# Performance work log

Hardware: AMD Instinct MI355X
Metric: run time of the kernel (lower is better)

The kernel has to match this reference:

```python
import jax, jax.numpy as jnp
import numpy as np

EPS = 1e-5

def layer_norm(x, gamma, beta):
    m = jnp.mean(x, axis=-1, keepdims=True)
    v = jnp.var(x, axis=-1, keepdims=True)
    return (x - m) / jnp.sqrt(v + EPS) * gamma + beta


def setup_inputs() -> dict:
    key = jax.random.key(0)
    ks = jax.random.split(key, 10)
    B, N, D = 2, 2048, 1024
    H, Dh = 16, 64
    C, CD = 256, 512
    inner = H * Dh  # 1024
    J = C + 1 + N  # 2305 = context + null + self

    x = jax.random.normal(ks[0], (B, N, D), dtype=jnp.float32)
    context = jax.random.normal(ks[1], (B, C, CD), dtype=jnp.float32)
    mask = jax.random.uniform(ks[2], (B, C + N)) < 0.9  # bool, mostly True
    attn_bias = jax.random.normal(ks[3], (H, N, J), dtype=jnp.float32) * 0.02

    norm_gamma = jnp.ones((D,), dtype=jnp.float32)
    null_kv = jax.random.normal(ks[4], (2, Dh), dtype=jnp.float32)
    Wq = jax.random.normal(ks[5], (D, inner), dtype=jnp.float32) * (D ** -0.5)
    Wkv = jax.random.normal(ks[6], (D, 2 * Dh), dtype=jnp.float32) * (D ** -0.5)
    ctx_ln_w = jnp.ones((CD,), dtype=jnp.float32)
    ctx_ln_b = jnp.zeros((CD,), dtype=jnp.float32)
    Wctx = jax.random.normal(ks[7], (CD, 2 * Dh), dtype=jnp.float32) * (CD ** -0.5)
    bctx = jnp.zeros((2 * Dh,), dtype=jnp.float32)
    Wout = jax.random.normal(ks[8], (inner, D), dtype=jnp.float32) * (inner ** -0.5)
    out_gamma = jnp.ones((D,), dtype=jnp.float32)

    return {"x": x, "context": context, "mask": mask, "attn_bias": attn_bias,
            "norm_gamma": norm_gamma, "null_kv": null_kv, "Wq": Wq, "Wkv": Wkv,
            "ctx_ln_w": ctx_ln_w, "ctx_ln_b": ctx_ln_b, "Wctx": Wctx, "bctx": bctx,
            "Wout": Wout, "out_gamma": out_gamma}


def reference(x, context, mask, attn_bias, norm_gamma, null_kv, Wq, Wkv,
              ctx_ln_w, ctx_ln_b, Wctx, bctx, Wout, out_gamma):
    B, N, D = x.shape
    Dh = null_kv.shape[-1]
    H = Wq.shape[-1] // Dh
    scale = Dh ** -0.5

    xn = layer_norm(x, norm_gamma, 0.0)
    q = (xn @ Wq).reshape(B, N, H, Dh).transpose(0, 2, 1, 3) * scale  # b h n d
    k, v = jnp.split(xn @ Wkv, 2, axis=-1)  # b n d each (multi-query: shared across heads)

    # prepend learned null kv token
    nk = jnp.broadcast_to(null_kv[0], (B, 1, Dh))
    nv = jnp.broadcast_to(null_kv[1], (B, 1, Dh))
    k = jnp.concatenate([nk, k], axis=1)
    v = jnp.concatenate([nv, v], axis=1)

    # prepend projected context tokens
    cn = layer_norm(context, ctx_ln_w, ctx_ln_b)
    ck, cv = jnp.split(cn @ Wctx + bctx, 2, axis=-1)
    k = jnp.concatenate([ck, k], axis=1)  # b j d, j = C + 1 + N
    v = jnp.concatenate([cv, v], axis=1)

    sim = jnp.einsum('bhid,bjd->bhij', q, k) + attn_bias
    # pad mask with True for the null token (left), then broadcast over h, i
    m = jnp.pad(mask, ((0, 0), (1, 0)), constant_values=True)[:, None, None, :]
    max_neg = -jnp.finfo(sim.dtype).max
    sim = jnp.where(m, sim, max_neg)

    attn = jax.nn.softmax(sim.astype(jnp.float32), axis=-1)
    out = jnp.einsum('bhij,bjd->bhid', attn, v)  # b h n d
    out = out.transpose(0, 2, 1, 3).reshape(B, N, H * Dh)
    return layer_norm(out @ Wout, out_gamma, 0.0)
```

## Files before the change

kernel.cpp:

```cpp
#include <hip/hip_runtime.h>

constexpr int B  = 2;
constexpr int N  = 2048;
constexpr int H  = 16;
constexpr int C  = 256;
constexpr int J  = C + 1 + N;
constexpr int Jp = 2368;
constexpr int NT = Jp / 64;
constexpr float EPS = 1e-5f;
constexpr float LOG2E = 1.4426950408889634f;

typedef __bf16 bf16x8 __attribute__((ext_vector_type(8)));
typedef float  f32x4  __attribute__((ext_vector_type(4)));
typedef unsigned int uint4v __attribute__((ext_vector_type(4)));
typedef __attribute__((address_space(3))) unsigned int lds_u32;
typedef const __attribute__((address_space(1))) unsigned int glb_u32;

__device__ inline void load_lds16(const void* g, void* l) {
    __builtin_amdgcn_global_load_lds((glb_u32*)g, (lds_u32*)l, 16, 0, 0);
}
__device__ inline unsigned short f2bf(float f) {
    unsigned int u = __builtin_bit_cast(unsigned int, f);
    u += 0x7fffu + ((u >> 16) & 1u);
    return (unsigned short)(u >> 16);
}
__device__ inline unsigned int packbf2(float a, float b) {
    union { __bf16 h[2]; unsigned int u; } cv;
    cv.h[0] = (__bf16)a;
    cv.h[1] = (__bf16)b;
    return cv.u;
}
__device__ inline float fexp2(float x) {
    float r;
    asm("v_exp_f32 %0, %1" : "=v"(r) : "v"(x));
    return r;
}
__device__ inline f32x4 mfma16(bf16x8 a, bf16x8 b, f32x4 c) {
    return __builtin_amdgcn_mfma_f32_16x16x32_bf16(a, b, c, 0, 0, 0);
}
__device__ inline f32x4 loadu4(const float* p) {
    f32x4 r;
    __builtin_memcpy(&r, p, 16);
    return r;
}

__global__ void mask_prep(const void* __restrict__ mraw, float* __restrict__ maskf) {
    __shared__ int bad_int, bad_f32;
    const int t = threadIdx.x;
    if (t == 0) { bad_int = 0; bad_f32 = 0; }
    __syncthreads();
    const unsigned int* w = (const unsigned int*)mraw;
    int li = 0, lf = 0;
    for (int i = t; i < 1152; i += 256) {
        unsigned int v = w[i];
        if (v > 1u) li = 1;
        if (v != 0u && v != 0x3F800000u) lf = 1;
    }
    if (li) atomicOr(&bad_int, 1);
    if (lf) atomicOr(&bad_f32, 1);
    __syncthreads();
    const int mode = (!bad_int) ? 0 : ((!bad_f32) ? 1 : 2);
    const unsigned char* bytes = (const unsigned char*)mraw;
    for (int i = t; i < 2 * Jp; i += 256) {
        const int b2 = i / Jp, jp = i - b2 * Jp;
        float v;
        if (jp == 0) v = 0.f;
        else if (jp >= J) v = -1e30f;
        else {
            const int idx = b2 * (C + N) + jp - 1;
            const int keep = (mode == 2) ? (bytes[idx] != 0) : (w[idx] != 0u);
            v = keep ? 0.f : -1e30f;
        }
        maskf[i] = v;
    }
}

__global__ void zero_pads(unsigned short* __restrict__ Kb, unsigned short* __restrict__ Vt) {
    const int t = threadIdx.x;
    for (int i = t; i < 2 * 63 * 64; i += 256) {
        const int b2 = i / (63 * 64);
        const int rr = (i / 64) % 63;
        const int d  = i % 64;
        Kb[(size_t)(b2 * Jp + J + rr) * 64 + d] = 0;
    }
    for (int i = t; i < 2 * 64 * 63; i += 256) {
        const int b2 = i / (64 * 63);
        const int d  = (i / 63) % 64;
        const int cc = i % 63;
        Vt[(size_t)(b2 * 64 + d) * Jp + J + cc] = 0;
    }
}

template <int BF16OUT>
__global__ void __launch_bounds__(256) ln1024(const float* __restrict__ x,
                                              const float* __restrict__ gamma,
                                              void* __restrict__ outp) {
    const int row = blockIdx.x;
    const int t = threadIdx.x;
    const float* xr = x + (size_t)row * 1024;
    float4 v = ((const float4*)xr)[t];
    float s  = v.x + v.y + v.z + v.w;
    float ss = v.x * v.x + v.y * v.y + v.z * v.z + v.w * v.w;
    #pragma unroll
    for (int o = 1; o < 64; o <<= 1) {
        s  += __shfl_xor(s, o);
        ss += __shfl_xor(ss, o);
    }
    __shared__ float red[8];
    const int w = t >> 6;
    if ((t & 63) == 0) { red[w * 2] = s; red[w * 2 + 1] = ss; }
    __syncthreads();
    s  = red[0] + red[2] + red[4] + red[6];
    ss = red[1] + red[3] + red[5] + red[7];
    const float mean = s * (1.0f / 1024.0f);
    const float var  = ss * (1.0f / 1024.0f) - mean * mean;
    const float rstd = rsqrtf(var + EPS);
    const float4 g = ((const float4*)gamma)[t];
    float o0 = (v.x - mean) * rstd * g.x;
    float o1 = (v.y - mean) * rstd * g.y;
    float o2 = (v.z - mean) * rstd * g.z;
    float o3 = (v.w - mean) * rstd * g.w;
    if (BF16OUT) {
        ushort4 u;
        u.x = f2bf(o0); u.y = f2bf(o1); u.z = f2bf(o2); u.w = f2bf(o3);
        *(ushort4*)((unsigned short*)outp + (size_t)row * 1024 + t * 4) = u;
    } else {
        *(float4*)((float*)outp + (size_t)row * 1024 + t * 4) = make_float4(o0, o1, o2, o3);
    }
}

__global__ void __launch_bounds__(256) transpose_w(const float* __restrict__ W,
                                                   unsigned short* __restrict__ WT,
                                                   int K, int Nn, float scale) {
    __shared__ float lds[64][68];
    const int k0 = blockIdx.x * 64, n0 = blockIdx.y * 64;
    const int t = threadIdx.x;
    const int kk = t >> 4, nn = (t & 15) * 4;
    #pragma unroll
    for (int r = 0; r < 4; r++) {
        const float4 v = *(const float4*)(W + (size_t)(k0 + kk + r * 16) * Nn + n0 + nn);
        lds[kk + r * 16][nn + 0] = v.x;
        lds[kk + r * 16][nn + 1] = v.y;
        lds[kk + r * 16][nn + 2] = v.z;
        lds[kk + r * 16][nn + 3] = v.w;
    }
    __syncthreads();
    const int nr = t >> 2, kc = (t & 3) * 16;
    #pragma unroll
    for (int u4 = 0; u4 < 4; u4++) {
        ushort4 u;
        u.x = f2bf(lds[kc + u4 * 4 + 0][nr] * scale);
        u.y = f2bf(lds[kc + u4 * 4 + 1][nr] * scale);
        u.z = f2bf(lds[kc + u4 * 4 + 2][nr] * scale);
        u.w = f2bf(lds[kc + u4 * 4 + 3][nr] * scale);
        *(ushort4*)(WT + (size_t)(n0 + nr) * K + k0 + kc + u4 * 4) = u;
    }
}

__global__ void __launch_bounds__(128) ctx_proj(const float* __restrict__ ctx,
                                                const float* __restrict__ lw,
                                                const float* __restrict__ lb,
                                                const float* __restrict__ Wc,
                                                const float* __restrict__ bc,
                                                unsigned short* __restrict__ Kb,
                                                unsigned short* __restrict__ Vt) {
    const int row = blockIdx.x;
    const int b2 = row >> 8, ci = row & 255;
    const int t = threadIdx.x;
    __shared__ float cn[512];
    __shared__ float red[4];
    const float* xr = ctx + (size_t)row * 512;
    float4 v = ((const float4*)xr)[t];
    float s  = v.x + v.y + v.z + v.w;
    float ss = v.x * v.x + v.y * v.y + v.z * v.z + v.w * v.w;
    #pragma unroll
    for (int o = 1; o < 64; o <<= 1) {
        s  += __shfl_xor(s, o);
        ss += __shfl_xor(ss, o);
    }
    const int w = t >> 6;
    if ((t & 63) == 0) { red[w * 2] = s; red[w * 2 + 1] = ss; }
    __syncthreads();
    s  = red[0] + red[2];
    ss = red[1] + red[3];
    const float mean = s * (1.0f / 512.0f);
    const float var  = ss * (1.0f / 512.0f) - mean * mean;
    const float rstd = rsqrtf(var + EPS);
    const float4 g  = ((const float4*)lw)[t];
    const float4 be = ((const float4*)lb)[t];
    float4 c4;
    c4.x = (v.x - mean) * rstd * g.x + be.x;
    c4.y = (v.y - mean) * rstd * g.y + be.y;
    c4.z = (v.z - mean) * rstd * g.z + be.z;
    c4.w = (v.w - mean) * rstd * g.w + be.w;
    *(float4*)&cn[t * 4] = c4;
    __syncthreads();
    float acc = bc[t];
    #pragma unroll 8
    for (int d = 0; d < 512; d++) acc = fmaf(cn[d], Wc[d * 128 + t], acc);
    const unsigned short bv = f2bf(acc);
    if (t < 64) Kb[(size_t)(b2 * Jp + ci) * 64 + t] = bv;
    else        Vt[(size_t)(b2 * 64 + (t - 64)) * Jp + ci] = bv;
}

__global__ void null_fill(const float* __restrict__ nkv,
                          unsigned short* __restrict__ Kb, unsigned short* __restrict__ Vt) {
    const int b2 = blockIdx.x;
    const int t = threadIdx.x;
    Kb[(size_t)(b2 * Jp + 256) * 64 + t] = f2bf(nkv[t]);
    Vt[(size_t)(b2 * 64 + t) * Jp + 256] = f2bf(nkv[64 + t]);
}

template <int MODE>
__global__ void __launch_bounds__(256, 2) gemm_bf16(
        const unsigned short* __restrict__ A, const unsigned short* __restrict__ BT,
        float* __restrict__ Cf, unsigned short* __restrict__ Cb,
        unsigned short* __restrict__ Kb, unsigned short* __restrict__ Vt,
        int M, int Nn, int K) {
    __shared__ __align__(16) unsigned char smem[65536];
    const int t = threadIdx.x;
    const int w = t >> 6, lane = t & 63;
    const int g = lane >> 4, ln15 = lane & 15;
    const int wm = w >> 1, wn = w & 1;
    const int row0 = blockIdx.x * 128, col0 = blockIdx.y * 128;
    const int nk = K >> 6;
    const int ls = lane >> 3;
    const int swz = (lane & 7) ^ ls;

    f32x4 acc[4][4];
    #pragma unroll
    for (int i = 0; i < 4; i++)
        #pragma unroll
        for (int jj = 0; jj < 4; jj++)
            acc[i][jj] = (f32x4){0.f, 0.f, 0.f, 0.f};

    auto stage = [&](int kt, int cur) {
        if (w < 2) {
            const unsigned short* src = A + (size_t)(row0 + w * 64 + ls) * K + kt * 64 + swz * 8;
            unsigned char* dst = smem + cur * 16384 + w * 8192;
            #pragma unroll
            for (int i = 0; i < 8; i++)
                load_lds16(src + (size_t)i * 8 * K, dst + i * 1024);
        } else {
            const unsigned short* src = BT + (size_t)(col0 + (w - 2) * 64 + ls) * K + kt * 64 + swz * 8;
            unsigned char* dst = smem + 32768 + cur * 16384 + (w - 2) * 8192;
            #pragma unroll
            for (int i = 0; i < 8; i++)
                load_lds16(src + (size_t)i * 8 * K, dst + i * 1024);
        }
    };

    stage(0, 0);
    __syncthreads();
    for (int kt = 0; kt < nk; kt++) {
        const int cur = kt & 1;
        if (kt + 1 < nk) stage(kt + 1, cur ^ 1);
        const unsigned char* As = smem + cur * 16384;
        const unsigned char* Bs = smem + 32768 + cur * 16384;
        #pragma unroll
        for (int ks = 0; ks < 2; ks++) {
            bf16x8 af[4], bf[4];
            #pragma unroll
            for (int mq = 0; mq < 4; mq++)
                af[mq] = *(const bf16x8*)(As + (wm * 64 + mq * 16 + ln15) * 128 +
                                          ((ks * 64 + g * 16) ^ ((ln15 & 7) << 4)));
            #pragma unroll
            for (int nq = 0; nq < 4; nq++)
                bf[nq] = *(const bf16x8*)(Bs + (wn * 64 + nq * 16 + ln15) * 128 +
                                          ((ks * 64 + g * 16) ^ ((ln15 & 7) << 4)));
            #pragma unroll
            for (int mq = 0; mq < 4; mq++)
                #pragma unroll
                for (int nq = 0; nq < 4; nq++)
                    acc[mq][nq] = mfma16(af[mq], bf[nq], acc[mq][nq]);
        }
        __syncthreads();
    }

    #pragma unroll
    for (int mq = 0; mq < 4; mq++) {
        #pragma unroll
        for (int nq = 0; nq < 4; nq++) {
            #pragma unroll
            for (int r = 0; r < 4; r++) {
                const int gr = row0 + wm * 64 + mq * 16 + g * 4 + r;
                const int gc = col0 + wn * 64 + nq * 16 + ln15;
                if (MODE == 0) {
                    Cf[(size_t)gr * Nn + gc] = acc[mq][nq][r];
                } else if (MODE == 1) {
                    Cb[(size_t)gr * Nn + gc] = f2bf(acc[mq][nq][r]);
                } else {
                    const int b2 = gr >> 11, tok = gr & 2047;
                    const unsigned short v = f2bf(acc[mq][nq][r]);
                    if (gc < 64) Kb[(size_t)(b2 * Jp + 257 + tok) * 64 + gc] = v;
                    else         Vt[(size_t)(b2 * 64 + gc - 64) * Jp + 257 + tok] = v;
                }
            }
        }
    }
}

__global__ void __launch_bounds__(1024, 4) attn_v8(
        const unsigned short* __restrict__ qb, const unsigned short* __restrict__ Kb,
        const unsigned short* __restrict__ Vt, const float* __restrict__ bias,
        const float* __restrict__ maskf, unsigned short* __restrict__ aout) {
    __shared__ __align__(16) unsigned char smem[135168];
    const int t = threadIdx.x;
    const int w = t >> 6, lane = t & 63;
    const int g = lane >> 4, ln15 = lane & 15;
    const int i0 = blockIdx.x * 128, h = blockIdx.y;
    const int b2 = w & 1, wq = w >> 1;
    const int ls = lane >> 3;
    const int swz = (lane & 7) ^ ls;

    auto stage = [&](int jt, int cur) {
        const int j0 = jt * 64;
        const int quarter = w & 3;
        if (w < 8) {
            const int kb = (w >> 2) & 1;
            const unsigned short* src = Kb + (size_t)(kb * Jp + j0 + quarter * 16 + ls) * 64 + swz * 8;
            unsigned char* dst = smem + cur * 32768 + kb * 8192 + quarter * 2048;
            load_lds16(src, dst);
            load_lds16(src + (size_t)8 * 64, dst + 1024);
        } else {
            const int vb = (w >> 2) & 1;
            const unsigned short* src = Vt + (size_t)(vb * 64 + quarter * 16 + ls) * Jp + j0 + swz * 8;
            unsigned char* dst = smem + cur * 32768 + 16384 + vb * 8192 + quarter * 2048;
            load_lds16(src, dst);
            load_lds16(src + (size_t)8 * Jp, dst + 1024);
        }
    };

    const int bq  = t >> 3;
    const int bs0 = t & 7;
    const float* biasQrow = bias + ((size_t)h * N + i0 + bq) * J;
    auto bias_issue = [&](int jt, f32x4& r0, f32x4& r1) {
        const int j0 = jt * 64;
        if (j0 + 64 <= J) {
            r0 = loadu4(biasQrow + j0 + bs0 * 4);
            r1 = loadu4(biasQrow + j0 + (bs0 + 8) * 4);
        } else {
            #pragma unroll
            for (int c = 0; c < 4; c++) {
                const int jA = j0 + bs0 * 4 + c;
                const int jB = j0 + (bs0 + 8) * 4 + c;
                r0[c] = (jA < J) ? biasQrow[jA] : 0.f;
                r1[c] = (jB < J) ? biasQrow[jB] : 0.f;
            }
        }
    };
    auto bias_write = [&](int cur, const f32x4& r0, const f32x4& r1) {
        float* basep = (float*)(smem + 65536 + cur * 34816) + bq * 68;
        *(f32x4*)(basep + bs0 * 4) = r0;
        *(f32x4*)(basep + (bs0 + 8) * 4) = r1;
    };

    bf16x8 qf[2];
    #pragma unroll
    for (int ks = 0; ks < 2; ks++)
        qf[ks] = *(const bf16x8*)(qb + (size_t)(b2 * N + i0 + wq * 16 + ln15) * 1024 +
                                  h * 64 + ks * 32 + g * 8);

    float mrun = -1e30f, lrun = 0.f;
    f32x4 outA[4];
    #pragma unroll
    for (int nq = 0; nq < 4; nq++) outA[nq] = (f32x4){0.f, 0.f, 0.f, 0.f};

    const int srclA = ln15 + (((2 * g + 0) & 3) << 4);
    const int srclB = ln15 + (((2 * g + 1) & 3) << 4);

    auto compute = [&](int jt, int cur) {
        const int j0 = jt * 64;
        const unsigned char* Kl = smem + cur * 32768 + b2 * 8192;
        const unsigned char* Vl = smem + cur * 32768 + 16384 + b2 * 8192;
        const float* bb = (const float*)(smem + 65536 + cur * 34816) + (wq * 16 + ln15) * 68;

        f32x4 mk[4];
        #pragma unroll
        for (int jqm = 0; jqm < 4; jqm++)
            mk[jqm] = *(const f32x4*)(maskf + b2 * Jp + j0 + jqm * 16 + g * 4);
        f32x4 br[4];
        #pragma unroll
        for (int jqm = 0; jqm < 4; jqm++)
            br[jqm] = *(const f32x4*)(bb + (jqm * 4 + g) * 4);

        f32x4 S[4];
        #pragma unroll
        for (int jqm = 0; jqm < 4; jqm++) S[jqm] = (f32x4){0.f, 0.f, 0.f, 0.f};
        #pragma unroll
        for (int ks = 0; ks < 2; ks++) {
            bf16x8 ka[4];
            #pragma unroll
            for (int jqm = 0; jqm < 4; jqm++)
                ka[jqm] = *(const bf16x8*)(Kl + (jqm * 16 + ln15) * 128 +
                                           ((ks * 64 + g * 16) ^ ((ln15 & 7) << 4)));
            __builtin_amdgcn_s_setprio(1);
            #pragma unroll
            for (int jqm = 0; jqm < 4; jqm++)
                S[jqm] = mfma16(ka[jqm], qf[ks], S[jqm]);
            __builtin_amdgcn_s_setprio(0);
        }

        float sv[4][4];
        #pragma unroll
        for (int jqm = 0; jqm < 4; jqm++)
            #pragma unroll
            for (int r = 0; r < 4; r++)
                sv[jqm][r] = fmaf(br[jqm][r], LOG2E, S[jqm][r]) + mk[jqm][r];

        float tmj[4];
        #pragma unroll
        for (int jqm = 0; jqm < 4; jqm++)
            tmj[jqm] = fmaxf(fmaxf(sv[jqm][0], sv[jqm][1]), fmaxf(sv[jqm][2], sv[jqm][3]));
        float tm = fmaxf(fmaxf(tmj[0], tmj[1]), fmaxf(tmj[2], tmj[3]));
        tm = fmaxf(tm, __shfl_xor(tm, 16));
        tm = fmaxf(tm, __shfl_xor(tm, 32));

        if (!__all(tm <= mrun)) {
            const float mnew = fmaxf(mrun, tm);
            const float cor = fexp2(mrun - mnew);
            mrun = mnew;
            float corr[4];
            #pragma unroll
            for (int r = 0; r < 4; r++) corr[r] = __shfl(cor, g * 4 + r, 64);
            #pragma unroll
            for (int nq = 0; nq < 4; nq++)
                #pragma unroll
                for (int r = 0; r < 4; r++)
                    outA[nq][r] *= corr[r];
            lrun *= cor;
        }
        const float mcur = mrun;

        float p[4][4];
        #pragma unroll
        for (int jqm = 0; jqm < 4; jqm++)
            #pragma unroll
            for (int r = 0; r < 4; r++)
                p[jqm][r] = fexp2(sv[jqm][r] - mcur);
        float tsj[4];
        #pragma unroll
        for (int jqm = 0; jqm < 4; jqm++)
            tsj[jqm] = (p[jqm][0] + p[jqm][1]) + (p[jqm][2] + p[jqm][3]);
        float ts = (tsj[0] + tsj[1]) + (tsj[2] + tsj[3]);
        ts += __shfl_xor(ts, 16);
        ts += __shfl_xor(ts, 32);
        lrun += ts;

        unsigned int Wp[4][2];
        #pragma unroll
        for (int jqm = 0; jqm < 4; jqm++) {
            Wp[jqm][0] = packbf2(p[jqm][0], p[jqm][1]);
            Wp[jqm][1] = packbf2(p[jqm][2], p[jqm][3]);
        }

        #pragma unroll
        for (int ks = 0; ks < 2; ks++) {
            uint4v wd;
            #pragma unroll
            for (int widx = 0; widx < 4; widx++) {
                const int srcl = (widx >> 1) ? srclB : srclA;
                const int t0 = __shfl((int)Wp[ks * 2 + 0][widx & 1], srcl, 64);
                const int t1 = __shfl((int)Wp[ks * 2 + 1][widx & 1], srcl, 64);
                wd[widx] = (unsigned int)((g >> 1) ? t1 : t0);
            }
            const bf16x8 pa = __builtin_bit_cast(bf16x8, wd);
            bf16x8 vf[4];
            #pragma unroll
            for (int nq = 0; nq < 4; nq++)
                vf[nq] = *(const bf16x8*)(Vl + (nq * 16 + ln15) * 128 +
                                          ((ks * 64 + g * 16) ^ ((ln15 & 7) << 4)));
            __builtin_amdgcn_s_setprio(1);
            #pragma unroll
            for (int nq = 0; nq < 4; nq++)
                outA[nq] = mfma16(pa, vf[nq], outA[nq]);
            __builtin_amdgcn_s_setprio(0);
        }
    };

    f32x4 bR0, bR1;
    bias_issue(0, bR0, bR1);
    stage(0, 0);
    bias_write(0, bR0, bR1);
    __syncthreads();
    for (int jt = 0; jt < NT; jt++) {
        const int cur = jt & 1;
        if (jt + 1 < NT) {
            bias_issue(jt + 1, bR0, bR1);
            stage(jt + 1, cur ^ 1);
        }
        compute(jt, cur);
        if (jt + 1 < NT) bias_write(cur ^ 1, bR0, bR1);
        __syncthreads();
    }

    const float inv = 1.0f / lrun;
    float invr[4];
    #pragma unroll
    for (int r = 0; r < 4; r++) invr[r] = __shfl(inv, g * 4 + r, 64);
    #pragma unroll
    for (int nq = 0; nq < 4; nq++)
        #pragma unroll
        for (int r = 0; r < 4; r++)
            aout[(size_t)(b2 * N + i0 + wq * 16 + g * 4 + r) * 1024 +
                 h * 64 + nq * 16 + ln15] = f2bf(outA[nq][r] * invr[r]);
}

extern "C" void kernel_launch(void* const* d_in, const int* in_sizes, int n_in,
                              void* d_out, int out_size, void* d_ws, size_t ws_size,
                              hipStream_t stream) {
    const float* x         = (const float*)d_in[0];
    const float* context   = (const float*)d_in[1];
    const void*  mask      = d_in[2];
    const float* bias      = (const float*)d_in[3];
    const float* norm_g    = (const float*)d_in[4];
    const float* null_kv   = (const float*)d_in[5];
    const float* Wq        = (const float*)d_in[6];
    const float* Wkv       = (const float*)d_in[7];
    const float* ctx_ln_w  = (const float*)d_in[8];
    const float* ctx_ln_b  = (const float*)d_in[9];
    const float* Wctx      = (const float*)d_in[10];
    const float* bctx      = (const float*)d_in[11];
    const float* Wout      = (const float*)d_in[12];
    const float* out_gamma = (const float*)d_in[13];
    float* out = (float*)d_out;

    unsigned char* wsb = (unsigned char*)d_ws;
    unsigned short* xnb   = (unsigned short*)(wsb + 0);
    unsigned short* qbb   = (unsigned short*)(wsb + 8388608);
    float*          y     = (float*)(wsb + 0);
    unsigned short* aoutp = (unsigned short*)(wsb + 16777216);
    unsigned short* KbP   = (unsigned short*)(wsb + 25165824);
    unsigned short* VtP   = (unsigned short*)(wsb + 25772032);
    float*          maskf = (float*)(wsb + 26378240);
    unsigned short* WqT   = (unsigned short*)(wsb + 26397184);
    unsigned short* WkvT  = (unsigned short*)(wsb + 28494336);
    unsigned short* WoutT = (unsigned short*)(wsb + 28756480);

    mask_prep<<<1, 256, 0, stream>>>(mask, maskf);
    zero_pads<<<1, 256, 0, stream>>>(KbP, VtP);
    ln1024<1><<<B * N, 256, 0, stream>>>(x, norm_g, xnb);
    transpose_w<<<dim3(16, 16), 256, 0, stream>>>(Wq, WqT, 1024, 1024, 0.125f * LOG2E);
    transpose_w<<<dim3(16, 2), 256, 0, stream>>>(Wkv, WkvT, 1024, 128, 1.0f);
    transpose_w<<<dim3(16, 16), 256, 0, stream>>>(Wout, WoutT, 1024, 1024, 1.0f);
    ctx_proj<<<B * C, 128, 0, stream>>>(context, ctx_ln_w, ctx_ln_b, Wctx, bctx, KbP, VtP);
    null_fill<<<B, 64, 0, stream>>>(null_kv, KbP, VtP);
    gemm_bf16<1><<<dim3(32, 8), 256, 0, stream>>>(xnb, WqT, nullptr, qbb, nullptr, nullptr, 4096, 1024, 1024);
    gemm_bf16<2><<<dim3(32, 1), 256, 0, stream>>>(xnb, WkvT, nullptr, nullptr, KbP, VtP, 4096, 128, 1024);
    attn_v8<<<dim3(16, 16), 1024, 0, stream>>>(qbb, KbP, VtP, bias, maskf, aoutp);
    gemm_bf16<0><<<dim3(32, 8), 256, 0, stream>>>(aoutp, WoutT, y, nullptr, nullptr, nullptr, 4096, 1024, 1024);
    ln1024<0><<<B * N, 256, 0, stream>>>(y, out_gamma, out);
}
```

Measured before the change: 252.2 us.

## Halve attention block to 8 waves, each wave processing two query tiles

The attention kernel now launches 512 threads instead of 1024, and each wave handles 32 query rows (two 16-row tiles) instead of 16. Each K and V fragment read from LDS feeds two MFMAs, and the staging and bias-load work is spread over fewer threads with more loads each. The aim is to cut LDS traffic per MFMA and raise per-wave instruction-level parallelism. In exchange it doubles accumulator and score register use per wave and halves the number of waves per block, which can reduce latency hiding.

Measured after the change: 273.6 us. 1.09x slower.

```diff
diff --git a/kernel.cpp b/kernel.cpp
--- a/kernel.cpp
+++ b/kernel.cpp
@@ -300,7 +300,7 @@
     }
 }
 
-__global__ void __launch_bounds__(1024, 4) attn_v8(
+__global__ void __launch_bounds__(512, 2) attn_v9(
         const unsigned short* __restrict__ qb, const unsigned short* __restrict__ Kb,
         const unsigned short* __restrict__ Vt, const float* __restrict__ bias,
         const float* __restrict__ maskf, unsigned short* __restrict__ aout) {
@@ -315,56 +315,71 @@
 
     auto stage = [&](int jt, int cur) {
         const int j0 = jt * 64;
-        const int quarter = w & 3;
-        if (w < 8) {
-            const int kb = (w >> 2) & 1;
-            const unsigned short* src = Kb + (size_t)(kb * Jp + j0 + quarter * 16 + ls) * 64 + swz * 8;
-            unsigned char* dst = smem + cur * 32768 + kb * 8192 + quarter * 2048;
-            load_lds16(src, dst);
-            load_lds16(src + (size_t)8 * 64, dst + 1024);
+        const int half = w & 1;
+        if (w < 4) {
+            const int kb = w >> 1;
+            const unsigned short* src = Kb + (size_t)(kb * Jp + j0 + half * 32 + ls) * 64 + swz * 8;
+            unsigned char* dst = smem + cur * 32768 + kb * 8192 + half * 4096;
+            #pragma unroll
+            for (int i = 0; i < 4; i++)
+                load_lds16(src + (size_t)i * 8 * 64, dst + i * 1024);
         } else {
-            const int vb = (w >> 2) & 1;
-            const unsigned short* src = Vt + (size_t)(vb * 64 + quarter * 16 + ls) * Jp + j0 + swz * 8;
-            unsigned char* dst = smem + cur * 32768 + 16384 + vb * 8192 + quarter * 2048;
-            load_lds16(src, dst);
-            load_lds16(src + (size_t)8 * Jp, dst + 1024);
+            const int vb = (w - 4) >> 1;
+            const unsigned short* src = Vt + (size_t)(vb * 64 + half * 32 + ls) * Jp + j0 + swz * 8;
+            unsigned char* dst = smem + cur * 32768 + 16384 + vb * 8192 + half * 4096;
+            #pragma unroll
+            for (int i = 0; i < 4; i++)
+                load_lds16(src + (size_t)i * 8 * Jp, dst + i * 1024);
         }
     };
 
-    const int bq  = t >> 3;
-    const int bs0 = t & 7;
+    const int bq  = t >> 2;
+    const int bs0 = (t & 3) * 16;
     const float* biasQrow = bias + ((size_t)h * N + i0 + bq) * J;
-    auto bias_issue = [&](int jt, f32x4& r0, f32x4& r1) {
+    auto bias_issue = [&](int jt, f32x4& r0, f32x4& r1, f32x4& r2, f32x4& r3) {
         const int j0 = jt * 64;
         if (j0 + 64 <= J) {
-            r0 = loadu4(biasQrow + j0 + bs0 * 4);
-            r1 = loadu4(biasQrow + j0 + (bs0 + 8) * 4);
+            r0 = loadu4(biasQrow + j0 + bs0 + 0);
+            r1 = loadu4(biasQrow + j0 + bs0 + 4);
+            r2 = loadu4(biasQrow + j0 + bs0 + 8);
+            r3 = loadu4(biasQrow + j0 + bs0 + 12);
         } else {
             #pragma unroll
             for (int c = 0; c < 4; c++) {
-                const int jA = j0 + bs0 * 4 + c;
-                const int jB = j0 + (bs0 + 8) * 4 + c;
-                r0[c] = (jA < J) ? biasQrow[jA] : 0.f;
-                r1[c] = (jB < J) ? biasQrow[jB] : 0.f;
+                const int ja = j0 + bs0 + c;
+                r0[c] = (ja      < J) ? biasQrow[ja]      : 0.f;
+                r1[c] = (ja + 4  < J) ? biasQrow[ja + 4]  : 0.f;
+                r2[c] = (ja + 8  < J) ? biasQrow[ja + 8]  : 0.f;
+                r3[c] = (ja + 12 < J) ? biasQrow[ja + 12] : 0.f;
             }
         }
     };
-    auto bias_write = [&](int cur, const f32x4& r0, const f32x4& r1) {
-        float* basep = (float*)(smem + 65536 + cur * 34816) + bq * 68;
-        *(f32x4*)(basep + bs0 * 4) = r0;
-        *(f32x4*)(basep + (bs0 + 8) * 4) = r1;
+    auto bias_write = [&](int cur, const f32x4& r0, const f32x4& r1,
+                          const f32x4& r2, const f32x4& r3) {
+        float* basep = (float*)(smem + 65536 + cur * 34816) + bq * 68 + bs0;
+        *(f32x4*)(basep + 0)  = r0;
+        *(f32x4*)(basep + 4)  = r1;
+        *(f32x4*)(basep + 8)  = r2;
+        *(f32x4*)(basep + 12) = r3;
     };
 
-    bf16x8 qf[2];
-    #pragma unroll
-    for (int ks = 0; ks < 2; ks++)
-        qf[ks] = *(const bf16x8*)(qb + (size_t)(b2 * N + i0 + wq * 16 + ln15) * 1024 +
-                                  h * 64 + ks * 32 + g * 8);
-
-    float mrun = -1e30f, lrun = 0.f;
-    f32x4 outA[4];
-    #pragma unroll
-    for (int nq = 0; nq < 4; nq++) outA[nq] = (f32x4){0.f, 0.f, 0.f, 0.f};
+    bf16x8 qf[2][2];
+    #pragma unroll
+    for (int qq = 0; qq < 2; qq++)
+        #pragma unroll
+        for (int ks = 0; ks < 2; ks++)
+            qf[qq][ks] = *(const bf16x8*)(qb +
+                (size_t)(b2 * N + i0 + wq * 32 + qq * 16 + ln15) * 1024 +
+                h * 64 + ks * 32 + g * 8);
+
+    float mrun[2] = {-1e30f, -1e30f};
+    float lrun[2] = {0.f, 0.f};
+    f32x4 outA[2][4];
+    #pragma unroll
+    for (int qq = 0; qq < 2; qq++)
+        #pragma unroll
+        for (int nq = 0; nq < 4; nq++)
+            outA[qq][nq] = (f32x4){0.f, 0.f, 0.f, 0.f};
 
     const int srclA = ln15 + (((2 * g + 0) & 3) << 4);
     const int srclB = ln15 + (((2 * g + 1) & 3) << 4);
@@ -373,20 +388,19 @@
         const int j0 = jt * 64;
         const unsigned char* Kl = smem + cur * 32768 + b2 * 8192;
         const unsigned char* Vl = smem + cur * 32768 + 16384 + b2 * 8192;
-        const float* bb = (const float*)(smem + 65536 + cur * 34816) + (wq * 16 + ln15) * 68;
+        const float* bbase = (const float*)(smem + 65536 + cur * 34816);
 
         f32x4 mk[4];
         #pragma unroll
         for (int jqm = 0; jqm < 4; jqm++)
             mk[jqm] = *(const f32x4*)(maskf + b2 * Jp + j0 + jqm * 16 + g * 4);
-        f32x4 br[4];
-        #pragma unroll
-        for (int jqm = 0; jqm < 4; jqm++)
-            br[jqm] = *(const f32x4*)(bb + (jqm * 4 + g) * 4);
-
-        f32x4 S[4];
-        #pragma unroll
-        for (int jqm = 0; jqm < 4; jqm++) S[jqm] = (f32x4){0.f, 0.f, 0.f, 0.f};
+
+        f32x4 S[2][4];
+        #pragma unroll
+        for (int qq = 0; qq < 2; qq++)
+            #pragma unroll
+            for (int jqm = 0; jqm < 4; jqm++)
+                S[qq][jqm] = (f32x4){0.f, 0.f, 0.f, 0.f};
         #pragma unroll
         for (int ks = 0; ks < 2; ks++) {
             bf16x8 ka[4];
@@ -396,75 +410,87 @@
                                            ((ks * 64 + g * 16) ^ ((ln15 & 7) << 4)));
             __builtin_amdgcn_s_setprio(1);
             #pragma unroll
-            for (int jqm = 0; jqm < 4; jqm++)
-                S[jqm] = mfma16(ka[jqm], qf[ks], S[jqm]);
+            for (int jqm = 0; jqm < 4; jqm++) {
+                S[0][jqm] = mfma16(ka[jqm], qf[0][ks], S[0][jqm]);
+                S[1][jqm] = mfma16(ka[jqm], qf[1][ks], S[1][jqm]);
+            }
             __builtin_amdgcn_s_setprio(0);
         }
 
-        float sv[4][4];
-        #pragma unroll
-        for (int jqm = 0; jqm < 4; jqm++)
-            #pragma unroll
-            for (int r = 0; r < 4; r++)
-                sv[jqm][r] = fmaf(br[jqm][r], LOG2E, S[jqm][r]) + mk[jqm][r];
-
-        float tmj[4];
-        #pragma unroll
-        for (int jqm = 0; jqm < 4; jqm++)
-            tmj[jqm] = fmaxf(fmaxf(sv[jqm][0], sv[jqm][1]), fmaxf(sv[jqm][2], sv[jqm][3]));
-        float tm = fmaxf(fmaxf(tmj[0], tmj[1]), fmaxf(tmj[2], tmj[3]));
-        tm = fmaxf(tm, __shfl_xor(tm, 16));
-        tm = fmaxf(tm, __shfl_xor(tm, 32));
-
-        if (!__all(tm <= mrun)) {
-            const float mnew = fmaxf(mrun, tm);
-            const float cor = fexp2(mrun - mnew);
-            mrun = mnew;
-            float corr[4];
-            #pragma unroll
-            for (int r = 0; r < 4; r++) corr[r] = __shfl(cor, g * 4 + r, 64);
-            #pragma unroll
-            for (int nq = 0; nq < 4; nq++)
+        unsigned int Wp[2][4][2];
+        #pragma unroll
+        for (int qq = 0; qq < 2; qq++) {
+            const float* bb = bbase + (wq * 32 + qq * 16 + ln15) * 68;
+            float sv[4][4];
+            #pragma unroll
+            for (int jqm = 0; jqm < 4; jqm++) {
+                const f32x4 br = *(const f32x4*)(bb + jqm * 16 + g * 4);
                 #pragma unroll
                 for (int r = 0; r < 4; r++)
-                    outA[nq][r] *= corr[r];
-            lrun *= cor;
-        }
-        const float mcur = mrun;
-
-        float p[4][4];
-        #pragma unroll
-        for (int jqm = 0; jqm < 4; jqm++)
-            #pragma unroll
-            for (int r = 0; r < 4; r++)
-                p[jqm][r] = fexp2(sv[jqm][r] - mcur);
-        float tsj[4];
-        #pragma unroll
-        for (int jqm = 0; jqm < 4; jqm++)
-            tsj[jqm] = (p[jqm][0] + p[jqm][1]) + (p[jqm][2] + p[jqm][3]);
-        float ts = (tsj[0] + tsj[1]) + (tsj[2] + tsj[3]);
-        ts += __shfl_xor(ts, 16);
-        ts += __shfl_xor(ts, 32);
-        lrun += ts;
-
-        unsigned int Wp[4][2];
-        #pragma unroll
-        for (int jqm = 0; jqm < 4; jqm++) {
-            Wp[jqm][0] = packbf2(p[jqm][0], p[jqm][1]);
-            Wp[jqm][1] = packbf2(p[jqm][2], p[jqm][3]);
+                    sv[jqm][r] = fmaf(br[r], LOG2E, S[qq][jqm][r]) + mk[jqm][r];
+            }
+
+            float tmj[4];
+            #pragma unroll
+            for (int jqm = 0; jqm < 4; jqm++)
+                tmj[jqm] = fmaxf(fmaxf(sv[jqm][0], sv[jqm][1]), fmaxf(sv[jqm][2], sv[jqm][3]));
+            float tm = fmaxf(fmaxf(tmj[0], tmj[1]), fmaxf(tmj[2], tmj[3]));
+            tm = fmaxf(tm, __shfl_xor(tm, 16));
+            tm = fmaxf(tm, __shfl_xor(tm, 32));
+
+            if (!__all(tm <= mrun[qq])) {
+                const float mnew = fmaxf(mrun[qq], tm);
+                const float cor = fexp2(mrun[qq] - mnew);
+                mrun[qq] = mnew;
+                float corr[4];
+                #pragma unroll
+                for (int r = 0; r < 4; r++) corr[r] = __shfl(cor, g * 4 + r, 64);
+                #pragma unroll
+                for (int nq = 0; nq < 4; nq++)
+                    #pragma unroll
+                    for (int r = 0; r < 4; r++)
+                        outA[qq][nq][r] *= corr[r];
+                lrun[qq] *= cor;
+            }
+            const float mcur = mrun[qq];
+
+            float p[4][4];
+            #pragma unroll
+            for (int jqm = 0; jqm < 4; jqm++)
+                #pragma unroll
+                for (int r = 0; r < 4; r++)
+                    p[jqm][r] = fexp2(sv[jqm][r] - mcur);
+            float tsj[4];
+            #pragma unroll
+            for (int jqm = 0; jqm < 4; jqm++)
+                tsj[jqm] = (p[jqm][0] + p[jqm][1]) + (p[jqm][2] + p[jqm][3]);
+            float ts = (tsj[0] + tsj[1]) + (tsj[2] + tsj[3]);
+            ts += __shfl_xor(ts, 16);
+            ts += __shfl_xor(ts, 32);
+            lrun[qq] += ts;
+
+            #pragma unroll
+            for (int jqm = 0; jqm < 4; jqm++) {
+                Wp[qq][jqm][0] = packbf2(p[jqm][0], p[jqm][1]);
+                Wp[qq][jqm][1] = packbf2(p[jqm][2], p[jqm][3]);
+            }
         }
 
         #pragma unroll
         for (int ks = 0; ks < 2; ks++) {
-            uint4v wd;
-            #pragma unroll
-            for (int widx = 0; widx < 4; widx++) {
-                const int srcl = (widx >> 1) ? srclB : srclA;
-                const int t0 = __shfl((int)Wp[ks * 2 + 0][widx & 1], srcl, 64);
-                const int t1 = __shfl((int)Wp[ks * 2 + 1][widx & 1], srcl, 64);
-                wd[widx] = (unsigned int)((g >> 1) ? t1 : t0);
-            }
-            const bf16x8 pa = __builtin_bit_cast(bf16x8, wd);
+            bf16x8 pa[2];
+            #pragma unroll
+            for (int qq = 0; qq < 2; qq++) {
+                uint4v wd;
+                #pragma unroll
+                for (int widx = 0; widx < 4; widx++) {
+                    const int srcl = (widx >> 1) ? srclB : srclA;
+                    const int t0 = __shfl((int)Wp[qq][ks * 2 + 0][widx & 1], srcl, 64);
+                    const int t1 = __shfl((int)Wp[qq][ks * 2 + 1][widx & 1], srcl, 64);
+                    wd[widx] = (unsigned int)((g >> 1) ? t1 : t0);
+                }
+                pa[qq] = __builtin_bit_cast(bf16x8, wd);
+            }
             bf16x8 vf[4];
             #pragma unroll
             for (int nq = 0; nq < 4; nq++)
@@ -472,38 +498,43 @@
                                           ((ks * 64 + g * 16) ^ ((ln15 & 7) << 4)));
             __builtin_amdgcn_s_setprio(1);
             #pragma unroll
-            for (int nq = 0; nq < 4; nq++)
-                outA[nq] = mfma16(pa, vf[nq], outA[nq]);
+            for (int nq = 0; nq < 4; nq++) {
+                outA[0][nq] = mfma16(pa[0], vf[nq], outA[0][nq]);
+                outA[1][nq] = mfma16(pa[1], vf[nq], outA[1][nq]);
+            }
             __builtin_amdgcn_s_setprio(0);
         }
     };
 
-    f32x4 bR0, bR1;
-    bias_issue(0, bR0, bR1);
+    f32x4 bR0, bR1, bR2, bR3;
+    bias_issue(0, bR0, bR1, bR2, bR3);
     stage(0, 0);
-    bias_write(0, bR0, bR1);
+    bias_write(0, bR0, bR1, bR2, bR3);
     __syncthreads();
     for (int jt = 0; jt < NT; jt++) {
         const int cur = jt & 1;
         if (jt + 1 < NT) {
-            bias_issue(jt + 1, bR0, bR1);
+            bias_issue(jt + 1, bR0, bR1, bR2, bR3);
             stage(jt + 1, cur ^ 1);
         }
         compute(jt, cur);
-        if (jt + 1 < NT) bias_write(cur ^ 1, bR0, bR1);
+        if (jt + 1 < NT) bias_write(cur ^ 1, bR0, bR1, bR2, bR3);
         __syncthreads();
     }
 
-    const float inv = 1.0f / lrun;
-    float invr[4];
-    #pragma unroll
-    for (int r = 0; r < 4; r++) invr[r] = __shfl(inv, g * 4 + r, 64);
-    #pragma unroll
-    for (int nq = 0; nq < 4; nq++)
-        #pragma unroll
-        for (int r = 0; r < 4; r++)
-            aout[(size_t)(b2 * N + i0 + wq * 16 + g * 4 + r) * 1024 +
-                 h * 64 + nq * 16 + ln15] = f2bf(outA[nq][r] * invr[r]);
+    #pragma unroll
+    for (int qq = 0; qq < 2; qq++) {
+        const float inv = 1.0f / lrun[qq];
+        float invr[4];
+        #pragma unroll
+        for (int r = 0; r < 4; r++) invr[r] = __shfl(inv, g * 4 + r, 64);
+        #pragma unroll
+        for (int nq = 0; nq < 4; nq++)
+            #pragma unroll
+            for (int r = 0; r < 4; r++)
+                aout[(size_t)(b2 * N + i0 + wq * 32 + qq * 16 + g * 4 + r) * 1024 +
+                     h * 64 + nq * 16 + ln15] = f2bf(outA[qq][nq][r] * invr[r]);
+    }
 }
 
 extern "C" void kernel_launch(void* const* d_in, const int* in_sizes, int n_in,
@@ -547,7 +578,7 @@
     null_fill<<<B, 64, 0, stream>>>(null_kv, KbP, VtP);
     gemm_bf16<1><<<dim3(32, 8), 256, 0, stream>>>(xnb, WqT, nullptr, qbb, nullptr, nullptr, 4096, 1024, 1024);
     gemm_bf16<2><<<dim3(32, 1), 256, 0, stream>>>(xnb, WkvT, nullptr, nullptr, KbP, VtP, 4096, 128, 1024);
-    attn_v8<<<dim3(16, 16), 1024, 0, stream>>>(qbb, KbP, VtP, bias, maskf, aoutp);
+    attn_v9<<<dim3(16, 16), 512, 0, stream>>>(qbb, KbP, VtP, bias, maskf, aoutp);
     gemm_bf16<0><<<dim3(32, 8), 256, 0, stream>>>(aoutp, WoutT, y, nullptr, nullptr, nullptr, 4096, 1024, 1024);
     ln1024<0><<<B * N, 256, 0, stream>>>(y, out_gamma, out);
 }
```

## Single-buffer attention LDS for two blocks per CU; merge small prep kernels

Applied to the files above, without the earlier changes.

The attention kernel drops its double-buffered K/V/bias staging in LDS and uses one buffer, halving shared memory so two 1024-thread blocks can be resident per CU. In exchange, loads for the next tile no longer overlap compute within a block, and an extra barrier is added per tile. Latency hiding now depends on the second resident block. Separately, the mask prep, pad zeroing and null-KV fill kernels are merged into one three-block launch to cut launch overhead.

New measurement: 770.3 us. +205.4%, slower.

```diff
diff --git a/kernel.cpp b/kernel.cpp
--- a/kernel.cpp
+++ b/kernel.cpp
@@ -44,50 +44,57 @@
     return r;
 }
 
-__global__ void mask_prep(const void* __restrict__ mraw, float* __restrict__ maskf) {
-    __shared__ int bad_int, bad_f32;
+__global__ void prep_all(const void* __restrict__ mraw, float* __restrict__ maskf,
+                         unsigned short* __restrict__ Kb, unsigned short* __restrict__ Vt,
+                         const float* __restrict__ nkv) {
     const int t = threadIdx.x;
-    if (t == 0) { bad_int = 0; bad_f32 = 0; }
-    __syncthreads();
-    const unsigned int* w = (const unsigned int*)mraw;
-    int li = 0, lf = 0;
-    for (int i = t; i < 1152; i += 256) {
-        unsigned int v = w[i];
-        if (v > 1u) li = 1;
-        if (v != 0u && v != 0x3F800000u) lf = 1;
-    }
-    if (li) atomicOr(&bad_int, 1);
-    if (lf) atomicOr(&bad_f32, 1);
-    __syncthreads();
-    const int mode = (!bad_int) ? 0 : ((!bad_f32) ? 1 : 2);
-    const unsigned char* bytes = (const unsigned char*)mraw;
-    for (int i = t; i < 2 * Jp; i += 256) {
-        const int b2 = i / Jp, jp = i - b2 * Jp;
-        float v;
-        if (jp == 0) v = 0.f;
-        else if (jp >= J) v = -1e30f;
-        else {
-            const int idx = b2 * (C + N) + jp - 1;
-            const int keep = (mode == 2) ? (bytes[idx] != 0) : (w[idx] != 0u);
-            v = keep ? 0.f : -1e30f;
-        }
-        maskf[i] = v;
-    }
-}
-
-__global__ void zero_pads(unsigned short* __restrict__ Kb, unsigned short* __restrict__ Vt) {
-    const int t = threadIdx.x;
-    for (int i = t; i < 2 * 63 * 64; i += 256) {
-        const int b2 = i / (63 * 64);
-        const int rr = (i / 64) % 63;
-        const int d  = i % 64;
-        Kb[(size_t)(b2 * Jp + J + rr) * 64 + d] = 0;
-    }
-    for (int i = t; i < 2 * 64 * 63; i += 256) {
-        const int b2 = i / (64 * 63);
-        const int d  = (i / 63) % 64;
-        const int cc = i % 63;
-        Vt[(size_t)(b2 * 64 + d) * Jp + J + cc] = 0;
+    if (blockIdx.x == 0) {
+        __shared__ int bad_int, bad_f32;
+        if (t == 0) { bad_int = 0; bad_f32 = 0; }
+        __syncthreads();
+        const unsigned int* w = (const unsigned int*)mraw;
+        int li = 0, lf = 0;
+        for (int i = t; i < 1152; i += 256) {
+            unsigned int v = w[i];
+            if (v > 1u) li = 1;
+            if (v != 0u && v != 0x3F800000u) lf = 1;
+        }
+        if (li) atomicOr(&bad_int, 1);
+        if (lf) atomicOr(&bad_f32, 1);
+        __syncthreads();
+        const int mode = (!bad_int) ? 0 : ((!bad_f32) ? 1 : 2);
+        const unsigned char* bytes = (const unsigned char*)mraw;
+        for (int i = t; i < 2 * Jp; i += 256) {
+            const int b2 = i / Jp, jp = i - b2 * Jp;
+            float v;
+            if (jp == 0) v = 0.f;
+            else if (jp >= J) v = -1e30f;
+            else {
+                const int idx = b2 * (C + N) + jp - 1;
+                const int keep = (mode == 2) ? (bytes[idx] != 0) : (w[idx] != 0u);
+                v = keep ? 0.f : -1e30f;
+            }
+            maskf[i] = v;
+        }
+    } else if (blockIdx.x == 1) {
+        for (int i = t; i < 2 * 63 * 64; i += 256) {
+            const int b2 = i / (63 * 64);
+            const int rr = (i / 64) % 63;
+            const int d  = i % 64;
+            Kb[(size_t)(b2 * Jp + J + rr) * 64 + d] = 0;
+        }
+        for (int i = t; i < 2 * 64 * 63; i += 256) {
+            const int b2 = i / (64 * 63);
+            const int d  = (i / 63) % 64;
+            const int cc = i % 63;
+            Vt[(size_t)(b2 * 64 + d) * Jp + J + cc] = 0;
+        }
+    } else {
+        if (t < 128) {
+            const int b2 = t >> 6, d = t & 63;
+            Kb[(size_t)(b2 * Jp + 256) * 64 + d] = f2bf(nkv[d]);
+            Vt[(size_t)(b2 * 64 + d) * Jp + 256] = f2bf(nkv[64 + d]);
+        }
     }
 }
 
@@ -203,14 +210,6 @@
     else        Vt[(size_t)(b2 * 64 + (t - 64)) * Jp + ci] = bv;
 }
 
-__global__ void null_fill(const float* __restrict__ nkv,
-                          unsigned short* __restrict__ Kb, unsigned short* __restrict__ Vt) {
-    const int b2 = blockIdx.x;
-    const int t = threadIdx.x;
-    Kb[(size_t)(b2 * Jp + 256) * 64 + t] = f2bf(nkv[t]);
-    Vt[(size_t)(b2 * 64 + t) * Jp + 256] = f2bf(nkv[64 + t]);
-}
-
 template <int MODE>
 __global__ void __launch_bounds__(256, 2) gemm_bf16(
         const unsigned short* __restrict__ A, const unsigned short* __restrict__ BT,
@@ -300,11 +299,11 @@
     }
 }
 
-__global__ void __launch_bounds__(1024, 4) attn_v8(
+__global__ void __launch_bounds__(1024, 8) attn_v13(
         const unsigned short* __restrict__ qb, const unsigned short* __restrict__ Kb,
         const unsigned short* __restrict__ Vt, const float* __restrict__ bias,
         const float* __restrict__ maskf, unsigned short* __restrict__ aout) {
-    __shared__ __align__(16) unsigned char smem[135168];
+    __shared__ __align__(16) unsigned char smem[67584];
     const int t = threadIdx.x;
     const int w = t >> 6, lane = t & 63;
     const int g = lane >> 4, ln15 = lane & 15;
@@ -313,19 +312,19 @@
     const int ls = lane >> 3;
     const int swz = (lane & 7) ^ ls;
 
-    auto stage = [&](int jt, int cur) {
+    auto stage = [&](int jt) {
         const int j0 = jt * 64;
         const int quarter = w & 3;
         if (w < 8) {
             const int kb = (w >> 2) & 1;
             const unsigned short* src = Kb + (size_t)(kb * Jp + j0 + quarter * 16 + ls) * 64 + swz * 8;
-            unsigned char* dst = smem + cur * 32768 + kb * 8192 + quarter * 2048;
+            unsigned char* dst = smem + kb * 8192 + quarter * 2048;
             load_lds16(src, dst);
             load_lds16(src + (size_t)8 * 64, dst + 1024);
         } else {
             const int vb = (w >> 2) & 1;
             const unsigned short* src = Vt + (size_t)(vb * 64 + quarter * 16 + ls) * Jp + j0 + swz * 8;
-            unsigned char* dst = smem + cur * 32768 + 16384 + vb * 8192 + quarter * 2048;
+            unsigned char* dst = smem + 16384 + vb * 8192 + quarter * 2048;
             load_lds16(src, dst);
             load_lds16(src + (size_t)8 * Jp, dst + 1024);
         }
@@ -349,8 +348,8 @@
             }
         }
     };
-    auto bias_write = [&](int cur, const f32x4& r0, const f32x4& r1) {
-        float* basep = (float*)(smem + 65536 + cur * 34816) + bq * 68;
+    auto bias_write = [&](const f32x4& r0, const f32x4& r1) {
+        float* basep = (float*)(smem + 32768) + bq * 68;
         *(f32x4*)(basep + bs0 * 4) = r0;
         *(f32x4*)(basep + (bs0 + 8) * 4) = r1;
     };
@@ -369,11 +368,11 @@
     const int srclA = ln15 + (((2 * g + 0) & 3) << 4);
     const int srclB = ln15 + (((2 * g + 1) & 3) << 4);
 
-    auto compute = [&](int jt, int cur) {
+    auto compute = [&](int jt) {
         const int j0 = jt * 64;
-        const unsigned char* Kl = smem + cur * 32768 + b2 * 8192;
-        const unsigned char* Vl = smem + cur * 32768 + 16384 + b2 * 8192;
-        const float* bb = (const float*)(smem + 65536 + cur * 34816) + (wq * 16 + ln15) * 68;
+        const unsigned char* Kl = smem + b2 * 8192;
+        const unsigned char* Vl = smem + 16384 + b2 * 8192;
+        const float* bb = (const float*)(smem + 32768) + (wq * 16 + ln15) * 68;
 
         f32x4 mk[4];
         #pragma unroll
@@ -478,19 +477,13 @@
         }
     };
 
-    f32x4 bR0, bR1;
-    bias_issue(0, bR0, bR1);
-    stage(0, 0);
-    bias_write(0, bR0, bR1);
-    __syncthreads();
     for (int jt = 0; jt < NT; jt++) {
-        const int cur = jt & 1;
-        if (jt + 1 < NT) {
-            bias_issue(jt + 1, bR0, bR1);
-            stage(jt + 1, cur ^ 1);
-        }
-        compute(jt, cur);
-        if (jt + 1 < NT) bias_write(cur ^ 1, bR0, bR1);
+        f32x4 bR0, bR1;
+        bias_issue(jt, bR0, bR1);
+        stage(jt);
+        bias_write(bR0, bR1);
+        __syncthreads();
+        compute(jt);
         __syncthreads();
     }
 
@@ -537,17 +530,15 @@
     unsigned short* WkvT  = (unsigned short*)(wsb + 28494336);
     unsigned short* WoutT = (unsigned short*)(wsb + 28756480);
 
-    mask_prep<<<1, 256, 0, stream>>>(mask, maskf);
-    zero_pads<<<1, 256, 0, stream>>>(KbP, VtP);
+    prep_all<<<3, 256, 0, stream>>>(mask, maskf, KbP, VtP, null_kv);
     ln1024<1><<<B * N, 256, 0, stream>>>(x, norm_g, xnb);
     transpose_w<<<dim3(16, 16), 256, 0, stream>>>(Wq, WqT, 1024, 1024, 0.125f * LOG2E);
     transpose_w<<<dim3(16, 2), 256, 0, stream>>>(Wkv, WkvT, 1024, 128, 1.0f);
     transpose_w<<<dim3(16, 16), 256, 0, stream>>>(Wout, WoutT, 1024, 1024, 1.0f);
     ctx_proj<<<B * C, 128, 0, stream>>>(context, ctx_ln_w, ctx_ln_b, Wctx, bctx, KbP, VtP);
-    null_fill<<<B, 64, 0, stream>>>(null_kv, KbP, VtP);
     gemm_bf16<1><<<dim3(32, 8), 256, 0, stream>>>(xnb, WqT, nullptr, qbb, nullptr, nullptr, 4096, 1024, 1024);
     gemm_bf16<2><<<dim3(32, 1), 256, 0, stream>>>(xnb, WkvT, nullptr, nullptr, KbP, VtP, 4096, 128, 1024);
-    attn_v8<<<dim3(16, 16), 1024, 0, stream>>>(qbb, KbP, VtP, bias, maskf, aoutp);
+    attn_v13<<<dim3(16, 16), 1024, 0, stream>>>(qbb, KbP, VtP, bias, maskf, aoutp);
     gemm_bf16<0><<<dim3(32, 8), 256, 0, stream>>>(aoutp, WoutT, y, nullptr, nullptr, nullptr, 4096, 1024, 1024);
     ln1024<0><<<B * N, 256, 0, stream>>>(y, out_gamma, out);
 }
```
